# Kernel tuning notes

Hardware: AMD Instinct MI355X
Metric: run time of the kernel (lower is better)

## Reference

```python
import jax, jax.numpy as jnp
import numpy as np

B, C, H, W = 16, 512, 32, 32
HID = 4 * C


def setup_inputs() -> dict:
    key = jax.random.key(0)
    k_x, k_w1, k_w2 = jax.random.split(key, 3)
    x = jax.random.normal(k_x, (B, C, H, W), dtype=jnp.float32)
    # 1x1 conv weights stored as [out, in] matrices (kernel_size=1)
    w1 = jax.random.normal(k_w1, (HID, C), dtype=jnp.float32) * (1.0 / np.sqrt(C))
    b1 = jnp.zeros((HID,), dtype=jnp.float32)
    w2 = jax.random.normal(k_w2, (C, HID), dtype=jnp.float32) * (1.0 / np.sqrt(HID))
    b2 = jnp.zeros((C,), dtype=jnp.float32)
    return {"x": x, "w1": w1, "b1": b1, "w2": w2, "b2": b2}


def reference(x, w1, b1, w2, b2):
    Bd, Cd, Hd, Wd = x.shape
    scale = Cd ** (-0.5)
    xf = x.reshape(Bd, Cd, Hd * Wd)          # [B, C, N]
    q = jnp.swapaxes(xf, -1, -2)              # [B, N, C]
    # full spatial self-attention: scores [B, N, N]
    attn = jax.nn.softmax(jnp.einsum('bnc,bcm->bnm', q, xf) * scale, axis=-1)
    out = jnp.einsum('bnm,bmc->bnc', attn, q)  # [B, N, C]
    # 1x1-conv FFN applied per spatial position
    h = jax.nn.relu(jnp.einsum('bnc,dc->bnd', out, w1) + b1)   # [B, N, 4C]
    y = jnp.einsum('bnd,cd->bnc', h, w2) + b2                  # [B, N, C]
    y = jnp.swapaxes(y, -1, -2).reshape(Bd, Cd, Hd, Wd)
    return y + x
```

## Files before the change

kernel.cpp:

```cpp
#include <hip/hip_runtime.h>

#define BATCH 16
#define CH    512
#define NSP   1024
#define HIDD  2048

typedef __bf16 bf16x8 __attribute__((ext_vector_type(8)));
typedef float floatx4 __attribute__((ext_vector_type(4)));

__device__ __forceinline__ float bf2f(unsigned short u) {
    union { unsigned int i; float f; } v; v.i = ((unsigned int)u) << 16; return v.f;
}
__device__ __forceinline__ unsigned short f2bf(float f) {
    union { float f; unsigned int i; } v; v.f = f;
    unsigned int i = v.i;
    return (unsigned short)((i + 0x7FFFu + ((i >> 16) & 1u)) >> 16);
}

__device__ __forceinline__ void gload16(const void* g, void* l) {
    __builtin_amdgcn_global_load_lds(
        (__attribute__((address_space(1))) unsigned int*)(g),
        (__attribute__((address_space(3))) unsigned int*)(l),
        16, 0, 0);
}
#define MEMFENCE asm volatile("" ::: "memory")

template<int EPI, int MAP, int DEPTH>
__global__ __launch_bounds__(256, (DEPTH == 2) ? 3 : 2)
void gemm_bt(const unsigned short* __restrict__ A,
             const unsigned short* __restrict__ Bm,
             void* __restrict__ Cout,
             int Nn, int K,
             long sAb, long sBb, long sCb,
             const float* __restrict__ bias, float scale,
             const float* __restrict__ resid)
{
    constexpr int NBUF = DEPTH + 1;
    __shared__ unsigned short sA[NBUF][128 * 32];
    __shared__ unsigned short sB[NBUF][128 * 32];

    const int tid  = threadIdx.x;
    const int lane = tid & 63;
    const int w    = tid >> 6;
    const int quad = lane >> 4;
    const int l15  = lane & 15;
    const int mw   = (w >> 1) * 64;
    const int nw   = (w & 1) * 64;

    const int F = blockIdx.x;
    int m0, n0, b;
    if constexpr (MAP == 0) {
        const int xcd = F & 7, s = F >> 3;
        b = xcd + ((s >> 6) << 3);
        const int j = s & 63; m0 = (j >> 3) << 7; n0 = (j & 7) << 7;
    } else if constexpr (MAP == 1) {
        const int xcd = F & 7, s = F >> 3;
        b = xcd + ((s >> 5) << 3);
        const int j = s & 31; m0 = (j >> 2) << 7; n0 = (j & 3) << 7;
    } else if constexpr (MAP == 3) {
        const int xcd = F & 7, s = F >> 3;
        b = 0; m0 = (s & 3) << 7; n0 = ((xcd << 4) + (s >> 2)) << 7;
    } else {
        const int xcd = F & 7, s = F >> 3;
        const int g  = s >> 6;
        const int nn = (s >> 2) & 15;
        const int mi = s & 3;
        b = 0;
        m0 = ((xcd << 4) + (g << 2) + mi) << 7;
        n0 = nn << 7;
    }

    A  += (size_t)b * sAb;
    Bm += (size_t)b * sBb;

    const int srow = lane >> 2;
    const int sg   = (lane & 3) ^ ((lane >> 3) & 3);
    const unsigned short* pA = A  + (size_t)(m0 + w * 32 + srow) * K + sg * 8;
    const unsigned short* pB = Bm + (size_t)(n0 + w * 32 + srow) * K + sg * 8;
    const size_t rowskip16 = (size_t)16 * K;
    const int woff = w * 1024;
    const int rslot = ((l15 >> 1) & 3);

    floatx4 acc[4][4];
#pragma unroll
    for (int i = 0; i < 4; i++)
#pragma unroll
        for (int j = 0; j < 4; j++) acc[i][j] = (floatx4){0.f, 0.f, 0.f, 0.f};

    const int nIter = K >> 5;
    const int kLast = K - 32;

#pragma unroll
    for (int d = 0; d < DEPTH; ++d) {
        unsigned short* dA = &sA[d][0] + woff;
        unsigned short* dB = &sB[d][0] + woff;
        gload16(pA + d * 32,             dA);
        gload16(pA + d * 32 + rowskip16, dA + 512);
        gload16(pB + d * 32,             dB);
        gload16(pB + d * 32 + rowskip16, dB + 512);
        MEMFENCE;
    }

    int bcur = 0, bpf = DEPTH;
    for (int it = 0; it < nIter; ++it) {
        if constexpr (DEPTH == 2)
            asm volatile("s_waitcnt vmcnt(4)\n\ts_barrier" ::: "memory");
        else
            asm volatile("s_waitcnt vmcnt(8)\n\ts_barrier" ::: "memory");

        const int kpf = (it + DEPTH) * 32 <= kLast ? (it + DEPTH) * 32 : kLast;
        unsigned short* dA = &sA[0][0] + bpf * 4096 + woff;
        unsigned short* dB = &sB[0][0] + bpf * 4096 + woff;
        gload16(pA + kpf,             dA);
        gload16(pA + kpf + rowskip16, dA + 512);
        gload16(pB + kpf,             dB);
        gload16(pB + kpf + rowskip16, dB + 512);
        MEMFENCE;

        const unsigned short* bufA = &sA[0][0] + bcur * 4096;
        const unsigned short* bufB = &sB[0][0] + bcur * 4096;
        bf16x8 af[4], bfr[4];
#pragma unroll
        for (int mi = 0; mi < 4; mi++)
            af[mi] = *(const bf16x8*)(bufA + (mw + mi * 16 + l15) * 32
                                      + (quad ^ rslot) * 8);
#pragma unroll
        for (int ni = 0; ni < 4; ni++)
            bfr[ni] = *(const bf16x8*)(bufB + (nw + ni * 16 + l15) * 32
                                       + (quad ^ rslot) * 8);
#pragma unroll
        for (int mi = 0; mi < 4; mi++)
#pragma unroll
            for (int ni = 0; ni < 4; ni++)
                acc[mi][ni] = __builtin_amdgcn_mfma_f32_16x16x32_bf16(
                    af[mi], bfr[ni], acc[mi][ni], 0, 0, 0);

        bcur = bcur == NBUF - 1 ? 0 : bcur + 1;
        bpf  = bpf  == NBUF - 1 ? 0 : bpf  + 1;
    }
    asm volatile("s_waitcnt vmcnt(0)" ::: "memory");

    if constexpr (EPI == 4) {
        float* Of = (float*)Cout;
#pragma unroll
        for (int ni = 0; ni < 4; ni++) {
            const int j  = n0 + nw + ni * 16 + l15;
            const int bb = j >> 10, ns = j & 1023;
            const size_t cbase = (size_t)bb * CH * NSP + ns;
#pragma unroll
            for (int mi = 0; mi < 4; mi++) {
                const int ibase = m0 + mw + mi * 16 + quad * 4;
#pragma unroll
                for (int r = 0; r < 4; r++) {
                    const int c = ibase + r;
                    const size_t a = cbase + (size_t)c * NSP;
                    Of[a] = acc[mi][ni][r] + bias[c] + resid[a];
                }
            }
        }
    } else {
        unsigned short* Cb = (unsigned short*)Cout + (size_t)b * sCb;
#pragma unroll
        for (int ni = 0; ni < 4; ni++) {
            const int n = n0 + nw + ni * 16 + l15;
            float bv = 0.f;
            if constexpr (EPI == 2) bv = bias[n];
#pragma unroll
            for (int mi = 0; mi < 4; mi++) {
                const int mbase = m0 + mw + mi * 16 + quad * 4;
#pragma unroll
                for (int r = 0; r < 4; r++) {
                    float v = acc[mi][ni][r];
                    if constexpr (EPI == 0) v *= scale;
                    if constexpr (EPI == 2) v = fmaxf(v + bv, 0.f);
                    Cb[(size_t)(mbase + r) * Nn + n] = f2bf(v);
                }
            }
        }
    }
}

__global__ __launch_bounds__(256)
void pack_x_kernel(const float* __restrict__ x,
                   unsigned short* __restrict__ Xbf,
                   unsigned short* __restrict__ XT)
{
    __shared__ float tile[32][33];
    const int tx = threadIdx.x, ty = threadIdx.y;
    const int n0 = blockIdx.x * 32, c0 = blockIdx.y * 32, b = blockIdx.z;
    const size_t base = (size_t)b * CH * NSP;
#pragma unroll
    for (int i = ty; i < 32; i += 8) {
        float v = x[base + (size_t)(c0 + i) * NSP + n0 + tx];
        tile[i][tx] = v;
        Xbf[base + (size_t)(c0 + i) * NSP + n0 + tx] = f2bf(v);
    }
    __syncthreads();
    const size_t tbase = (size_t)b * NSP * CH;
#pragma unroll
    for (int i = ty; i < 32; i += 8)
        XT[tbase + (size_t)(n0 + i) * CH + c0 + tx] = f2bf(tile[tx][i]);
}

__global__ __launch_bounds__(256)
void cast_bf16_kernel(const float* __restrict__ src,
                      unsigned short* __restrict__ dst, int n)
{
    int i = blockIdx.x * 256 + threadIdx.x;
    if (i < n) dst[i] = f2bf(src[i]);
}

__global__ __launch_bounds__(256)
void softmax_kernel(unsigned short* __restrict__ S)
{
    const int row = blockIdx.x;
    unsigned short* p = S + (size_t)row * NSP;
    const int t = threadIdx.x;

    ushort4 u = ((const ushort4*)p)[t];
    float v0 = bf2f(u.x), v1 = bf2f(u.y), v2 = bf2f(u.z), v3 = bf2f(u.w);

    float m = fmaxf(fmaxf(v0, v1), fmaxf(v2, v3));
#pragma unroll
    for (int off = 32; off > 0; off >>= 1) m = fmaxf(m, __shfl_xor(m, off));
    __shared__ float redmax[4], redsum[4];
    const int wid = t >> 6;
    if ((t & 63) == 0) redmax[wid] = m;
    __syncthreads();
    m = fmaxf(fmaxf(redmax[0], redmax[1]), fmaxf(redmax[2], redmax[3]));

    v0 = __expf(v0 - m); v1 = __expf(v1 - m);
    v2 = __expf(v2 - m); v3 = __expf(v3 - m);
    float s = v0 + v1 + v2 + v3;
#pragma unroll
    for (int off = 32; off > 0; off >>= 1) s += __shfl_xor(s, off);
    if ((t & 63) == 0) redsum[wid] = s;
    __syncthreads();
    s = redsum[0] + redsum[1] + redsum[2] + redsum[3];

    const float inv = 1.0f / s;
    ushort4 o;
    o.x = f2bf(v0 * inv); o.y = f2bf(v1 * inv);
    o.z = f2bf(v2 * inv); o.w = f2bf(v3 * inv);
    ((ushort4*)p)[t] = o;
}

extern "C" void kernel_launch(void* const* d_in, const int* in_sizes, int n_in,
                              void* d_out, int out_size, void* d_ws, size_t ws_size,
                              hipStream_t stream)
{
    const float* x  = (const float*)d_in[0];
    const float* w1 = (const float*)d_in[1];
    const float* b1 = (const float*)d_in[2];
    const float* w2 = (const float*)d_in[3];
    const float* b2 = (const float*)d_in[4];
    float* out = (float*)d_out;

    char* ws = (char*)d_ws;
    unsigned short* Xbf = (unsigned short*)ws; ws += (size_t)BATCH * CH * NSP * 2;
    unsigned short* XT  = (unsigned short*)ws; ws += (size_t)BATCH * NSP * CH * 2;
    unsigned short* W1b = (unsigned short*)ws; ws += (size_t)HIDD * CH * 2;
    unsigned short* W2b = (unsigned short*)ws; ws += (size_t)CH * HIDD * 2;
    unsigned short* P   = (unsigned short*)ws; ws += (size_t)BATCH * NSP * NSP * 2;
    unsigned short* O   = (unsigned short*)ws; ws += (size_t)BATCH * NSP * CH * 2;
    unsigned short* Hb  = (unsigned short*)ws; ws += (size_t)BATCH * NSP * HIDD * 2;

    const dim3 blk(256);

    pack_x_kernel<<<dim3(NSP / 32, CH / 32, BATCH), dim3(32, 8), 0, stream>>>(x, Xbf, XT);
    cast_bf16_kernel<<<dim3((HIDD * CH) / 256), blk, 0, stream>>>(w1, W1b, HIDD * CH);
    cast_bf16_kernel<<<dim3((CH * HIDD) / 256), blk, 0, stream>>>(w2, W2b, CH * HIDD);

    gemm_bt<0, 0, 2><<<dim3(1024), blk, 0, stream>>>(
        XT, XT, P, NSP, CH,
        (long)NSP * CH, (long)NSP * CH, (long)NSP * NSP, nullptr,
        0.04419417382415922f, nullptr);

    softmax_kernel<<<dim3(BATCH * NSP), blk, 0, stream>>>(P);

    gemm_bt<1, 1, 2><<<dim3(512), blk, 0, stream>>>(
        P, Xbf, O, CH, NSP,
        (long)NSP * NSP, (long)CH * NSP, (long)NSP * CH, nullptr, 1.f, nullptr);

    gemm_bt<2, 5, 2><<<dim3(2048), blk, 0, stream>>>(
        O, W1b, Hb, HIDD, CH, 0, 0, 0, b1, 1.f, nullptr);

    gemm_bt<4, 3, 3><<<dim3(512), blk, 0, stream>>>(
        W2b, Hb, out, BATCH * NSP, HIDD, 0, 0, 0, b2, 1.f, x);
}
```

Measured before the change: 276.6 us.

## Add dedicated 256x128-tile FFN1 GEMM kernel with triple-buffered LDS pipeline

```diff
diff --git a/kernel.cpp b/kernel.cpp
--- a/kernel.cpp
+++ b/kernel.cpp
@@ -57,17 +57,9 @@
         const int xcd = F & 7, s = F >> 3;
         b = xcd + ((s >> 5) << 3);
         const int j = s & 31; m0 = (j >> 2) << 7; n0 = (j & 3) << 7;
-    } else if constexpr (MAP == 3) {
+    } else {
         const int xcd = F & 7, s = F >> 3;
         b = 0; m0 = (s & 3) << 7; n0 = ((xcd << 4) + (s >> 2)) << 7;
-    } else {
-        const int xcd = F & 7, s = F >> 3;
-        const int g  = s >> 6;
-        const int nn = (s >> 2) & 15;
-        const int mi = s & 3;
-        b = 0;
-        m0 = ((xcd << 4) + (g << 2) + mi) << 7;
-        n0 = nn << 7;
     }
 
     A  += (size_t)b * sAb;
@@ -163,8 +155,6 @@
 #pragma unroll
         for (int ni = 0; ni < 4; ni++) {
             const int n = n0 + nw + ni * 16 + l15;
-            float bv = 0.f;
-            if constexpr (EPI == 2) bv = bias[n];
 #pragma unroll
             for (int mi = 0; mi < 4; mi++) {
                 const int mbase = m0 + mw + mi * 16 + quad * 4;
@@ -172,10 +162,115 @@
                 for (int r = 0; r < 4; r++) {
                     float v = acc[mi][ni][r];
                     if constexpr (EPI == 0) v *= scale;
-                    if constexpr (EPI == 2) v = fmaxf(v + bv, 0.f);
                     Cb[(size_t)(mbase + r) * Nn + n] = f2bf(v);
                 }
             }
+        }
+    }
+}
+
+__global__ __launch_bounds__(256, 2)
+void ffn1_big(const unsigned short* __restrict__ A,
+              const unsigned short* __restrict__ Bm,
+              unsigned short* __restrict__ Cout,
+              const float* __restrict__ bias)
+{
+    const int K = CH, Nn = HIDD;
+    __shared__ unsigned short sA[3][256 * 32];
+    __shared__ unsigned short sB[3][128 * 32];
+
+    const int tid  = threadIdx.x;
+    const int lane = tid & 63;
+    const int w    = tid >> 6;
+    const int quad = lane >> 4;
+    const int l15  = lane & 15;
+    const int mw   = (w >> 1) * 128;
+    const int nw   = (w & 1) * 64;
+
+    const int F = blockIdx.x;
+    const int m0 = (F >> 4) << 8;
+    const int n0 = (F & 15) << 7;
+
+    const int srow = lane >> 2;
+    const int sg   = (lane & 3) ^ ((lane >> 3) & 3);
+    const unsigned short* pA = A  + (size_t)(m0 + w * 64 + srow) * K + sg * 8;
+    const unsigned short* pB = Bm + (size_t)(n0 + w * 32 + srow) * K + sg * 8;
+    const size_t rowskip16 = (size_t)16 * K;
+    const int woffA = w * 2048;
+    const int woffB = w * 1024;
+    const int rslot = ((l15 >> 1) & 3);
+
+    floatx4 acc[8][4];
+#pragma unroll
+    for (int i = 0; i < 8; i++)
+#pragma unroll
+        for (int j = 0; j < 4; j++) acc[i][j] = (floatx4){0.f, 0.f, 0.f, 0.f};
+
+    const int nIter = K >> 5;
+    const int kLast = K - 32;
+
+#pragma unroll
+    for (int d = 0; d < 2; ++d) {
+        unsigned short* dA = &sA[d][0] + woffA;
+        unsigned short* dB = &sB[d][0] + woffB;
+        gload16(pA + d * 32,                 dA);
+        gload16(pA + d * 32 +     rowskip16, dA + 512);
+        gload16(pA + d * 32 + 2 * rowskip16, dA + 1024);
+        gload16(pA + d * 32 + 3 * rowskip16, dA + 1536);
+        gload16(pB + d * 32,                 dB);
+        gload16(pB + d * 32 +     rowskip16, dB + 512);
+        MEMFENCE;
+    }
+
+    int bcur = 0, bpf = 2;
+    for (int it = 0; it < nIter; ++it) {
+        asm volatile("s_waitcnt vmcnt(6)\n\ts_barrier" ::: "memory");
+
+        const int kpf = (it + 2) * 32 <= kLast ? (it + 2) * 32 : kLast;
+        unsigned short* dA = &sA[0][0] + bpf * 8192 + woffA;
+        unsigned short* dB = &sB[0][0] + bpf * 4096 + woffB;
+        gload16(pA + kpf,                 dA);
+        gload16(pA + kpf +     rowskip16, dA + 512);
+        gload16(pA + kpf + 2 * rowskip16, dA + 1024);
+        gload16(pA + kpf + 3 * rowskip16, dA + 1536);
+        gload16(pB + kpf,                 dB);
+        gload16(pB + kpf +     rowskip16, dB + 512);
+        MEMFENCE;
+
+        const unsigned short* bufA = &sA[0][0] + bcur * 8192;
+        const unsigned short* bufB = &sB[0][0] + bcur * 4096;
+        bf16x8 af[8], bfr[4];
+#pragma unroll
+        for (int mi = 0; mi < 8; mi++)
+            af[mi] = *(const bf16x8*)(bufA + (mw + mi * 16 + l15) * 32
+                                      + (quad ^ rslot) * 8);
+#pragma unroll
+        for (int ni = 0; ni < 4; ni++)
+            bfr[ni] = *(const bf16x8*)(bufB + (nw + ni * 16 + l15) * 32
+                                       + (quad ^ rslot) * 8);
+#pragma unroll
+        for (int mi = 0; mi < 8; mi++)
+#pragma unroll
+            for (int ni = 0; ni < 4; ni++)
+                acc[mi][ni] = __builtin_amdgcn_mfma_f32_16x16x32_bf16(
+                    af[mi], bfr[ni], acc[mi][ni], 0, 0, 0);
+
+        bcur = bcur == 2 ? 0 : bcur + 1;
+        bpf  = bpf  == 2 ? 0 : bpf  + 1;
+    }
+    asm volatile("s_waitcnt vmcnt(0)" ::: "memory");
+
+#pragma unroll
+    for (int ni = 0; ni < 4; ni++) {
+        const int n = n0 + nw + ni * 16 + l15;
+        const float bv = bias[n];
+#pragma unroll
+        for (int mi = 0; mi < 8; mi++) {
+            const int mbase = m0 + mw + mi * 16 + quad * 4;
+#pragma unroll
+            for (int r = 0; r < 4; r++)
+                Cout[(size_t)(mbase + r) * Nn + n] =
+                    f2bf(fmaxf(acc[mi][ni][r] + bv, 0.f));
         }
     }
 }
@@ -282,8 +377,7 @@
         P, Xbf, O, CH, NSP,
         (long)NSP * NSP, (long)CH * NSP, (long)NSP * CH, nullptr, 1.f, nullptr);
 
-    gemm_bt<2, 5, 2><<<dim3(2048), blk, 0, stream>>>(
-        O, W1b, Hb, HIDD, CH, 0, 0, 0, b1, 1.f, nullptr);
+    ffn1_big<<<dim3(1024), blk, 0, stream>>>(O, W1b, Hb, b1);
 
     gemm_bt<4, 3, 3><<<dim3(512), blk, 0, stream>>>(
         W2b, Hb, out, BATCH * NSP, HIDD, 0, 0, 0, b2, 1.f, x);
```

Result: slower. 282.7 us (+2.2%).

## Fuse softmax into QK^T epilogue with deferred row normalization in PV GEMM

Applied to the files above, without the earlier changes.

```diff
diff --git a/kernel.cpp b/kernel.cpp
--- a/kernel.cpp
+++ b/kernel.cpp
@@ -33,7 +33,8 @@
              int Nn, int K,
              long sAb, long sBb, long sCb,
              const float* __restrict__ bias, float scale,
-             const float* __restrict__ resid)
+             const float* __restrict__ resid,
+             float* __restrict__ aux)
 {
     constexpr int NBUF = DEPTH + 1;
     __shared__ unsigned short sA[NBUF][128 * 32];
@@ -57,17 +58,11 @@
         const int xcd = F & 7, s = F >> 3;
         b = xcd + ((s >> 5) << 3);
         const int j = s & 31; m0 = (j >> 2) << 7; n0 = (j & 3) << 7;
-    } else if constexpr (MAP == 3) {
+    } else if constexpr (MAP == 2) {
+        b = 0; m0 = (F >> 4) << 7; n0 = (F & 15) << 7;
+    } else {
         const int xcd = F & 7, s = F >> 3;
         b = 0; m0 = (s & 3) << 7; n0 = ((xcd << 4) + (s >> 2)) << 7;
-    } else {
-        const int xcd = F & 7, s = F >> 3;
-        const int g  = s >> 6;
-        const int nn = (s >> 2) & 15;
-        const int mi = s & 3;
-        b = 0;
-        m0 = ((xcd << 4) + (g << 2) + mi) << 7;
-        n0 = nn << 7;
     }
 
     A  += (size_t)b * sAb;
@@ -143,41 +138,105 @@
     if constexpr (EPI == 4) {
         float* Of = (float*)Cout;
 #pragma unroll
-        for (int ni = 0; ni < 4; ni++) {
-            const int j  = n0 + nw + ni * 16 + l15;
-            const int bb = j >> 10, ns = j & 1023;
-            const size_t cbase = (size_t)bb * CH * NSP + ns;
+        for (int mi = 0; mi < 4; mi++) {
+#pragma unroll
+            for (int r = 0; r < 4; r++) {
+                const int c = m0 + mw + mi * 16 + quad * 4 + r;
+                const float bv = bias[c];
+#pragma unroll
+                for (int ni = 0; ni < 4; ni++) {
+                    const int j  = n0 + nw + ni * 16 + l15;
+                    const int bb = j >> 10, ns = j & 1023;
+                    const size_t a = (size_t)bb * CH * NSP + (size_t)c * NSP + ns;
+                    Of[a] = acc[mi][ni][r] + bv + resid[a];
+                }
+            }
+        }
+    } else if constexpr (EPI == 5) {
+#pragma unroll
+        for (int mi = 0; mi < 4; mi++)
+#pragma unroll
+            for (int ni = 0; ni < 4; ni++)
+#pragma unroll
+                for (int r = 0; r < 4; r++)
+                    acc[mi][ni][r] = __expf(acc[mi][ni][r] * scale);
+        {
+            const int chunk = (n0 + nw) >> 6;
+            float* ps = aux + (size_t)b * NSP * 16;
 #pragma unroll
             for (int mi = 0; mi < 4; mi++) {
-                const int ibase = m0 + mw + mi * 16 + quad * 4;
 #pragma unroll
                 for (int r = 0; r < 4; r++) {
-                    const int c = ibase + r;
-                    const size_t a = cbase + (size_t)c * NSP;
-                    Of[a] = acc[mi][ni][r] + bias[c] + resid[a];
+                    float s = acc[mi][0][r] + acc[mi][1][r]
+                            + acc[mi][2][r] + acc[mi][3][r];
+                    s += __shfl_xor(s, 1);
+                    s += __shfl_xor(s, 2);
+                    s += __shfl_xor(s, 4);
+                    s += __shfl_xor(s, 8);
+                    if (l15 == 0)
+                        ps[(size_t)(m0 + mw + mi * 16 + quad * 4 + r) * 16
+                           + chunk] = s;
                 }
+            }
+        }
+        unsigned short* Cb = (unsigned short*)Cout + (size_t)b * sCb;
+#pragma unroll
+        for (int mi = 0; mi < 4; mi++) {
+#pragma unroll
+            for (int r = 0; r < 4; r++) {
+                const size_t rowoff =
+                    (size_t)(m0 + mw + mi * 16 + quad * 4 + r) * Nn;
+#pragma unroll
+                for (int ni = 0; ni < 4; ni++)
+                    Cb[rowoff + n0 + nw + ni * 16 + l15] =
+                        f2bf(acc[mi][ni][r]);
+            }
+        }
+    } else if constexpr (EPI == 6) {
+        const float* invp = aux + (size_t)b * NSP;
+        unsigned short* Cb = (unsigned short*)Cout + (size_t)b * sCb;
+#pragma unroll
+        for (int mi = 0; mi < 4; mi++) {
+#pragma unroll
+            for (int r = 0; r < 4; r++) {
+                const int row = m0 + mw + mi * 16 + quad * 4 + r;
+                const float iv = invp[row];
+                const size_t rowoff = (size_t)row * Nn;
+#pragma unroll
+                for (int ni = 0; ni < 4; ni++)
+                    Cb[rowoff + n0 + nw + ni * 16 + l15] =
+                        f2bf(acc[mi][ni][r] * iv);
             }
         }
     } else {
         unsigned short* Cb = (unsigned short*)Cout + (size_t)b * sCb;
-#pragma unroll
-        for (int ni = 0; ni < 4; ni++) {
-            const int n = n0 + nw + ni * 16 + l15;
-            float bv = 0.f;
-            if constexpr (EPI == 2) bv = bias[n];
-#pragma unroll
-            for (int mi = 0; mi < 4; mi++) {
-                const int mbase = m0 + mw + mi * 16 + quad * 4;
-#pragma unroll
-                for (int r = 0; r < 4; r++) {
-                    float v = acc[mi][ni][r];
-                    if constexpr (EPI == 0) v *= scale;
-                    if constexpr (EPI == 2) v = fmaxf(v + bv, 0.f);
-                    Cb[(size_t)(mbase + r) * Nn + n] = f2bf(v);
-                }
-            }
-        }
-    }
+        float bv[4];
+#pragma unroll
+        for (int ni = 0; ni < 4; ni++) bv[ni] = bias[n0 + nw + ni * 16 + l15];
+#pragma unroll
+        for (int mi = 0; mi < 4; mi++) {
+#pragma unroll
+            for (int r = 0; r < 4; r++) {
+                const size_t rowoff =
+                    (size_t)(m0 + mw + mi * 16 + quad * 4 + r) * Nn;
+#pragma unroll
+                for (int ni = 0; ni < 4; ni++)
+                    Cb[rowoff + n0 + nw + ni * 16 + l15] =
+                        f2bf(fmaxf(acc[mi][ni][r] + bv[ni], 0.f));
+            }
+        }
+    }
+}
+
+__global__ __launch_bounds__(256)
+void rowsum_inv_kernel(const float* __restrict__ ps, float* __restrict__ inv)
+{
+    const int i = blockIdx.x * 256 + threadIdx.x;
+    const float* p = ps + (size_t)i * 16;
+    float s = 0.f;
+#pragma unroll
+    for (int k = 0; k < 16; k++) s += p[k];
+    inv[i] = 1.0f / s;
 }
 
 __global__ __launch_bounds__(256)
@@ -208,41 +267,6 @@
 {
     int i = blockIdx.x * 256 + threadIdx.x;
     if (i < n) dst[i] = f2bf(src[i]);
-}
-
-__global__ __launch_bounds__(256)
-void softmax_kernel(unsigned short* __restrict__ S)
-{
-    const int row = blockIdx.x;
-    unsigned short* p = S + (size_t)row * NSP;
-    const int t = threadIdx.x;
-
-    ushort4 u = ((const ushort4*)p)[t];
-    float v0 = bf2f(u.x), v1 = bf2f(u.y), v2 = bf2f(u.z), v3 = bf2f(u.w);
-
-    float m = fmaxf(fmaxf(v0, v1), fmaxf(v2, v3));
-#pragma unroll
-    for (int off = 32; off > 0; off >>= 1) m = fmaxf(m, __shfl_xor(m, off));
-    __shared__ float redmax[4], redsum[4];
-    const int wid = t >> 6;
-    if ((t & 63) == 0) redmax[wid] = m;
-    __syncthreads();
-    m = fmaxf(fmaxf(redmax[0], redmax[1]), fmaxf(redmax[2], redmax[3]));
-
-    v0 = __expf(v0 - m); v1 = __expf(v1 - m);
-    v2 = __expf(v2 - m); v3 = __expf(v3 - m);
-    float s = v0 + v1 + v2 + v3;
-#pragma unroll
-    for (int off = 32; off > 0; off >>= 1) s += __shfl_xor(s, off);
-    if ((t & 63) == 0) redsum[wid] = s;
-    __syncthreads();
-    s = redsum[0] + redsum[1] + redsum[2] + redsum[3];
-
-    const float inv = 1.0f / s;
-    ushort4 o;
-    o.x = f2bf(v0 * inv); o.y = f2bf(v1 * inv);
-    o.z = f2bf(v2 * inv); o.w = f2bf(v3 * inv);
-    ((ushort4*)p)[t] = o;
 }
 
 extern "C" void kernel_launch(void* const* d_in, const int* in_sizes, int n_in,
@@ -264,6 +288,8 @@
     unsigned short* P   = (unsigned short*)ws; ws += (size_t)BATCH * NSP * NSP * 2;
     unsigned short* O   = (unsigned short*)ws; ws += (size_t)BATCH * NSP * CH * 2;
     unsigned short* Hb  = (unsigned short*)ws; ws += (size_t)BATCH * NSP * HIDD * 2;
+    float*          Ps  = (float*)ws;          ws += (size_t)BATCH * NSP * 16 * 4;
+    float*          Inv = (float*)ws;          ws += (size_t)BATCH * NSP * 4;
 
     const dim3 blk(256);
 
@@ -271,20 +297,21 @@
     cast_bf16_kernel<<<dim3((HIDD * CH) / 256), blk, 0, stream>>>(w1, W1b, HIDD * CH);
     cast_bf16_kernel<<<dim3((CH * HIDD) / 256), blk, 0, stream>>>(w2, W2b, CH * HIDD);
 
-    gemm_bt<0, 0, 2><<<dim3(1024), blk, 0, stream>>>(
+    gemm_bt<5, 0, 2><<<dim3(1024), blk, 0, stream>>>(
         XT, XT, P, NSP, CH,
         (long)NSP * CH, (long)NSP * CH, (long)NSP * NSP, nullptr,
-        0.04419417382415922f, nullptr);
-
-    softmax_kernel<<<dim3(BATCH * NSP), blk, 0, stream>>>(P);
-
-    gemm_bt<1, 1, 2><<<dim3(512), blk, 0, stream>>>(
+        0.04419417382415922f, nullptr, Ps);
+
+    rowsum_inv_kernel<<<dim3(BATCH * NSP / 256), blk, 0, stream>>>(Ps, Inv);
+
+    gemm_bt<6, 1, 2><<<dim3(512), blk, 0, stream>>>(
         P, Xbf, O, CH, NSP,
-        (long)NSP * NSP, (long)CH * NSP, (long)NSP * CH, nullptr, 1.f, nullptr);
-
-    gemm_bt<2, 5, 2><<<dim3(2048), blk, 0, stream>>>(
-        O, W1b, Hb, HIDD, CH, 0, 0, 0, b1, 1.f, nullptr);
+        (long)NSP * NSP, (long)CH * NSP, (long)NSP * CH, nullptr, 1.f,
+        nullptr, Inv);
+
+    gemm_bt<2, 2, 3><<<dim3(2048), blk, 0, stream>>>(
+        O, W1b, Hb, HIDD, CH, 0, 0, 0, b1, 1.f, nullptr, nullptr);
 
     gemm_bt<4, 3, 3><<<dim3(512), blk, 0, stream>>>(
-        W2b, Hb, out, BATCH * NSP, HIDD, 0, 0, 0, b2, 1.f, x);
-}
+        W2b, Hb, out, BATCH * NSP, HIDD, 0, 0, 0, b2, 1.f, x, nullptr);
+}
```

Result: no change. 277.8 us (+0.4%).
